# Optimization experiments

Measured on AMD Instinct MI355X. Metric: run time of the kernel, lower is better.

The kernel has to match this reference:

```python
import jax, jax.numpy as jnp
import numpy as np

B, S, D, H = 2, 4096, 512, 8
HD = D // H  # head_dim = 64


def setup_inputs() -> dict:
    key = jax.random.key(0)
    ks = jax.random.split(key, 12)
    scale = 0.02
    inp = {
        "q": jax.random.normal(ks[0], (B, S, D), dtype=jnp.float32),
        "k": jax.random.normal(ks[1], (B, S, D), dtype=jnp.float32),
        "v": jax.random.normal(ks[2], (B, S, D), dtype=jnp.float32),
        "mask": jax.random.randint(ks[3], (B, S, S), 0, 2, dtype=jnp.int32),
        "wq_kernel": jax.random.normal(ks[4], (D, D), dtype=jnp.float32) * scale,
        "wq_bias": jnp.zeros((D,), dtype=jnp.float32),
        "wk_kernel": jax.random.normal(ks[5], (D, D), dtype=jnp.float32) * scale,
        "wk_bias": jnp.zeros((D,), dtype=jnp.float32),
        "wv_kernel": jax.random.normal(ks[6], (D, D), dtype=jnp.float32) * scale,
        "wv_bias": jnp.zeros((D,), dtype=jnp.float32),
        "wo_kernel": jax.random.normal(ks[7], (D, D), dtype=jnp.float32) * scale,
        "wo_bias": jnp.zeros((D,), dtype=jnp.float32),
    }
    return inp


def reference(q, k, v, mask, wq_kernel, wq_bias, wk_kernel, wk_bias,
              wv_kernel, wv_bias, wo_kernel, wo_bias):
    # Dense projections
    qp = q @ wq_kernel + wq_bias            # [B,S,D]
    kp = k @ wk_kernel + wk_bias
    vp = v @ wv_kernel + wv_bias

    def split_heads(x):
        # [B,S,D] -> [B,H,S,HD]
        return x.reshape(B, S, H, HD).transpose(0, 2, 1, 3)

    qh, kh, vh = split_heads(qp), split_heads(kp), split_heads(vp)

    # Scaled dot-product attention (materializes full [B,H,S,S] scores,
    # faithful to the original unfused implementation's math)
    scores = jnp.einsum('bhqd,bhkd->bhqk', qh, kh) / jnp.sqrt(
        jnp.asarray(HD, dtype=jnp.float32))
    scores = scores + mask.astype(jnp.float32)[:, None, :, :] * (-1e9)
    attn = jax.nn.softmax(scores, axis=-1)
    out = jnp.einsum('bhqk,bhkd->bhqd', attn, vh)   # [B,H,S,HD]

    # merge heads: [B,H,S,HD] -> [B,S,D]
    out = out.transpose(0, 2, 1, 3).reshape(B, S, D)
    return out @ wo_kernel + wo_bias
```

## Files before the change

kernel.cpp:

```cpp
#include <hip/hip_runtime.h>
#include <stdint.h>

#define B_ 2
#define S_ 4096
#define D_ 512
#define H_ 8
#define HD_ 64
#define M_ (B_*S_)

typedef __attribute__((ext_vector_type(8))) short bf16x8;
typedef __attribute__((ext_vector_type(4))) float f32x4;

#define QSCALE (0.125f * 1.44269504088896341f)
#define MFMA16(A,B,C) __builtin_amdgcn_mfma_f32_16x16x32_bf16((A),(B),(C),0,0,0)

__device__ __forceinline__ unsigned short f2bf(float f) {
  union { float f; unsigned u; } un; un.f = f;
  unsigned u = un.u;
  return (unsigned short)((u + 0x7fffu + ((u >> 16) & 1u)) >> 16);
}

__device__ __forceinline__ unsigned cvtpk(float lo, float hi) {
  unsigned r;
  asm("v_cvt_pk_bf16_f32 %0, %1, %2" : "=v"(r) : "v"(lo), "v"(hi));
  return r;
}

__device__ __forceinline__ void gl16(const void* g, void* l) {
  __builtin_amdgcn_global_load_lds(
      (const __attribute__((address_space(1))) void*)g,
      (__attribute__((address_space(3))) void*)l, 16, 0, 0);
}

__device__ __forceinline__ int kperm_inv(int p) {
  return ((p & 0x1C) << 1) | ((p & 0x20) >> 3) | (p & 3);
}

__global__ __launch_bounds__(256) void wtrans4(const float* __restrict__ w0, const float* __restrict__ w1,
                                               const float* __restrict__ w2, const float* __restrict__ w3,
                                               unsigned short* __restrict__ t0, unsigned short* __restrict__ t1,
                                               unsigned short* __restrict__ t2, unsigned short* __restrict__ t3) {
  const float* W = blockIdx.z==0?w0: blockIdx.z==1?w1: blockIdx.z==2?w2:w3;
  unsigned short* T = blockIdx.z==0?t0: blockIdx.z==1?t1: blockIdx.z==2?t2:t3;
  __shared__ float tile[32][33];
  int n0 = blockIdx.x*32, k0 = blockIdx.y*32;
  int tx = threadIdx.x & 31, ty = threadIdx.x >> 5;
  #pragma unroll
  for (int i=0;i<4;i++)
    tile[ty + i*8][tx] = W[(size_t)(k0 + ty + i*8)*D_ + n0 + tx];
  __syncthreads();
  #pragma unroll
  for (int i=0;i<4;i++)
    T[(size_t)(n0 + ty + i*8)*D_ + k0 + tx] = f2bf(tile[tx][ty + i*8]);
}

template<int OUT_MODE, int CONVA>
__device__ __forceinline__ void gemm_body(const void* __restrict__ Ap,
                                          const unsigned short* __restrict__ Wt,
                                          const float* __restrict__ bias,
                                          void* __restrict__ Out, float oscale) {
  __shared__ __align__(16) unsigned short lAB[2*128*64];
  unsigned short* lA = lAB;
  unsigned short* lB = lAB + 128*64;
  int bm = blockIdx.x, bn = blockIdx.y;
  int tid = threadIdx.x, lane = tid & 63, wid = tid >> 6;
  int g = lane >> 4, cc = lane & 15;
  int wm = wid >> 1, wn = wid & 1;

  f32x4 acc[4][4];
  #pragma unroll
  for (int mi=0;mi<4;mi++)
    #pragma unroll
    for (int ni=0;ni<4;ni++)
      acc[mi][ni] = (f32x4){0.f,0.f,0.f,0.f};

  for (int ks = 0; ks < D_; ks += 64) {
    __syncthreads();
    #pragma unroll
    for (int c4 = 0; c4 < 4; c4++) {
      int idx = wid*256 + c4*64 + lane;
      int row = idx >> 3, ch = idx & 7;
      int sw = ch ^ (row & 7);
      bf16x8 va;
      if (CONVA) {
        const float* a32 = (const float*)Ap + (size_t)(bm*128 + row)*D_ + ks + ch*8;
        float4 f0 = *(const float4*)a32;
        float4 f1 = *(const float4*)(a32 + 4);
        union { unsigned d[4]; bf16x8 v; } u;
        u.d[0] = cvtpk(f0.x, f0.y);
        u.d[1] = cvtpk(f0.z, f0.w);
        u.d[2] = cvtpk(f1.x, f1.y);
        u.d[3] = cvtpk(f1.z, f1.w);
        va = u.v;
      } else {
        va = *(const bf16x8*)((const unsigned short*)Ap + (size_t)(bm*128 + row)*D_ + ks + ch*8);
      }
      bf16x8 vb = *(const bf16x8*)(Wt + (size_t)(bn*128 + row)*D_ + ks + ch*8);
      *(bf16x8*)((char*)lA + row*128 + sw*16) = va;
      *(bf16x8*)((char*)lB + row*128 + sw*16) = vb;
    }
    __syncthreads();
    #pragma unroll
    for (int kk = 0; kk < 2; kk++) {
      bf16x8 af[4], bfv[4];
      #pragma unroll
      for (int mi=0;mi<4;mi++) {
        int row = wm*64 + mi*16 + cc;
        af[mi] = *(const bf16x8*)((const char*)lA + row*128 + (((4*kk+g) ^ (row&7))<<4));
      }
      #pragma unroll
      for (int ni=0;ni<4;ni++) {
        int row = wn*64 + ni*16 + cc;
        bfv[ni] = *(const bf16x8*)((const char*)lB + row*128 + (((4*kk+g) ^ (row&7))<<4));
      }
      #pragma unroll
      for (int mi=0;mi<4;mi++)
        #pragma unroll
        for (int ni=0;ni<4;ni++)
          acc[mi][ni] = MFMA16(af[mi], bfv[ni], acc[mi][ni]);
    }
  }

  if (OUT_MODE == 2) {
    __syncthreads();
    char* ldsT = (char*)lAB + wid*8192;
    #pragma unroll
    for (int ni=0;ni<4;ni++) {
      int n_l = ni*16 + cc;
      float bv = bias[bn*128 + wn*64 + n_l];
      #pragma unroll
      for (int mi=0;mi<4;mi++) {
        ushort4 pk;
        pk.x = f2bf(acc[mi][ni][0] + bv);
        pk.y = f2bf(acc[mi][ni][1] + bv);
        pk.z = f2bf(acc[mi][ni][2] + bv);
        pk.w = f2bf(acc[mi][ni][3] + bv);
        *(ushort4*)(ldsT + n_l*128 + ((32*mi + 8*g) ^ ((n_l&7)<<4))) = pk;
      }
    }
    asm volatile("s_waitcnt lgkmcnt(0)" ::: "memory");
    __builtin_amdgcn_sched_barrier(0);
    #pragma unroll
    for (int it=0; it<8; ++it) {
      int task = it*64 + lane;
      int row = task >> 3, ch = task & 7;
      bf16x8 vv = *(const bf16x8*)(ldsT + row*128 + ((ch ^ (row&7))<<4));
      int n_g = bn*128 + wn*64 + row;
      int m_g = bm*128 + wm*64 + ch*8;
      int bb = m_g >> 12, ss = m_g & (S_-1);
      int hh = n_g >> 6, hd = n_g & 63;
      *(bf16x8*)((unsigned short*)Out + (((size_t)(bb*H_+hh)*HD_ + hd)*S_ + ss)) = vv;
    }
    return;
  }

  #pragma unroll
  for (int ni=0;ni<4;ni++) {
    int n = bn*128 + wn*64 + ni*16 + cc;
    float bv = bias[n];
    #pragma unroll
    for (int mi=0;mi<4;mi++) {
      f32x4 vacc = acc[mi][ni];
      #pragma unroll
      for (int j=0;j<4;j++) {
        int r = bm*128 + wm*64 + mi*16 + 4*g + j;
        float val = (vacc[j] + bv) * oscale;
        if (OUT_MODE == 0) {
          int b = r >> 12, s = r & (S_-1);
          int h = n >> 6, hd = n & 63;
          ((unsigned short*)Out)[(((size_t)(b*H_ + h)*S_ + s) << 6) + hd] = f2bf(val);
        } else {
          ((float*)Out)[(size_t)r*D_ + n] = val;
        }
      }
    }
  }
}

__global__ __launch_bounds__(256,3) void qkv_gemm(
    const float* __restrict__ q32, const float* __restrict__ k32, const float* __restrict__ v32,
    const unsigned short* __restrict__ wqt, const unsigned short* __restrict__ wkt,
    const unsigned short* __restrict__ wvt,
    const float* __restrict__ bq, const float* __restrict__ bk, const float* __restrict__ bv,
    unsigned short* __restrict__ Qp, unsigned short* __restrict__ Kp,
    unsigned short* __restrict__ Vt,
    const int* __restrict__ mask, unsigned long long* __restrict__ bits) {
  if (blockIdx.z == 0) {
    const int lin = blockIdx.x + (blockIdx.y << 6);
    const int wid = threadIdx.x >> 6, lane = threadIdx.x & 63;
    const int wave_g = lin*4 + wid;
    const int* mp = mask + (size_t)wave_g*512*64 + lane;
    unsigned long long* bp = bits + (size_t)wave_g*512;
    #pragma unroll 1
    for (int it = 0; it < 64; ++it) {
      int m0 = mp[(it*8+0)*64]; int m1 = mp[(it*8+1)*64];
      int m2 = mp[(it*8+2)*64]; int m3 = mp[(it*8+3)*64];
      int m4 = mp[(it*8+4)*64]; int m5 = mp[(it*8+5)*64];
      int m6 = mp[(it*8+6)*64]; int m7 = mp[(it*8+7)*64];
      unsigned long long b0 = __ballot(m0 != 0);
      unsigned long long b1 = __ballot(m1 != 0);
      unsigned long long b2 = __ballot(m2 != 0);
      unsigned long long b3 = __ballot(m3 != 0);
      unsigned long long b4 = __ballot(m4 != 0);
      unsigned long long b5 = __ballot(m5 != 0);
      unsigned long long b6 = __ballot(m6 != 0);
      unsigned long long b7 = __ballot(m7 != 0);
      if (lane == 0) {
        bp[it*8+0] = b0; bp[it*8+1] = b1; bp[it*8+2] = b2; bp[it*8+3] = b3;
        bp[it*8+4] = b4; bp[it*8+5] = b5; bp[it*8+6] = b6; bp[it*8+7] = b7;
      }
    }
    return;
  }
  if (blockIdx.z == 1)      gemm_body<0,1>(q32, wqt, bq, Qp, QSCALE);
  else if (blockIdx.z == 2) gemm_body<0,1>(k32, wkt, bk, Kp, 1.0f);
  else                      gemm_body<2,1>(v32, wvt, bv, Vt, 1.0f);
}

__global__ __launch_bounds__(256,3) void o_gemm(const unsigned short* __restrict__ att,
                                                const unsigned short* __restrict__ wot,
                                                const float* __restrict__ bo,
                                                float* __restrict__ out) {
  gemm_body<1,0>(att, wot, bo, out, 1.0f);
}


#define WAITBAR { asm volatile("s_waitcnt vmcnt(6)" ::: "memory"); \
                  __builtin_amdgcn_s_barrier(); }

#define ISSUE(SLOT, TIDX) { \
    int tn_ = (TIDX) < NT ? (TIDX) : NT-1; \
    char* kb_ = lds + (SLOT)*8192 + woff; \
    char* vb_ = lds + 32768 + (SLOT)*8192 + woff; \
    gl16(gkA + (size_t)tn_*(64*HD_), kb_); \
    gl16(gkB + (size_t)tn_*(64*HD_), kb_ + 4096); \
    gl16(gvA + tn_*64, vb_); \
    gl16(gvB + tn_*64, vb_ + 4096); \
    msk0[SLOT] = mb0p[tn_]; \
    msk1[SLOT] = mb1p[tn_]; }

#define QK(SLOT, S0, S1) { \
    __builtin_amdgcn_s_setprio(1); \
    _Pragma("unroll") \
    for (int t4=0;t4<4;t4++) { \
      bf16x8 ak0 = *(const bf16x8*)(lds + (SLOT)*8192 + rdO[t4][0]); \
      bf16x8 ak1 = *(const bf16x8*)(lds + (SLOT)*8192 + rdO[t4][1]); \
      f32x4 s0 = (f32x4){0.f,0.f,0.f,0.f}; \
      s0 = MFMA16(ak0, aq00, s0); \
      s0 = MFMA16(ak1, aq01, s0); \
      f32x4 s1 = (f32x4){0.f,0.f,0.f,0.f}; \
      s1 = MFMA16(ak0, aq10, s1); \
      s1 = MFMA16(ak1, aq11, s1); \
      S0[t4] = s0; S1[t4] = s1; \
    } \
    __builtin_amdgcn_s_setprio(0); }

#define SMPV(S0, S1, VSLOT, MSLOT) { \
    unsigned long long sh0 = msk0[MSLOT] >> g8, sh1 = msk1[MSLOT] >> g8; \
    unsigned lo0=(unsigned)sh0, hi0=(unsigned)(sh0>>32); \
    unsigned lo1=(unsigned)sh1, hi1=(unsigned)(sh1>>32); \
    union { unsigned d[2][4]; bf16x8 v[2]; } P0_, P1_; \
    _Pragma("unroll") \
    for (int t4=0;t4<4;t4++) { \
      unsigned bm0=(t4&1)?hi0:lo0, bm1=(t4&1)?hi1:lo1; \
      const int bb=(t4>>1)*4; \
      float a0=__builtin_amdgcn_exp2f(S0[t4][0]-mj); \
      float a1=__builtin_amdgcn_exp2f(S0[t4][1]-mj); \
      float a2=__builtin_amdgcn_exp2f(S0[t4][2]-mj); \
      float a3=__builtin_amdgcn_exp2f(S0[t4][3]-mj); \
      a0=(bm0&(1u<<(bb+0)))?0.f:a0; a1=(bm0&(1u<<(bb+1)))?0.f:a1; \
      a2=(bm0&(1u<<(bb+2)))?0.f:a2; a3=(bm0&(1u<<(bb+3)))?0.f:a3; \
      P0_.d[t4&1][(t4>>1)*2]   = cvtpk(a0,a1); \
      P0_.d[t4&1][(t4>>1)*2+1] = cvtpk(a2,a3); \
      float c0=__builtin_amdgcn_exp2f(S1[t4][0]-mj); \
      float c1=__builtin_amdgcn_exp2f(S1[t4][1]-mj); \
      float c2=__builtin_amdgcn_exp2f(S1[t4][2]-mj); \
      float c3=__builtin_amdgcn_exp2f(S1[t4][3]-mj); \
      c0=(bm1&(1u<<(bb+0)))?0.f:c0; c1=(bm1&(1u<<(bb+1)))?0.f:c1; \
      c2=(bm1&(1u<<(bb+2)))?0.f:c2; c3=(bm1&(1u<<(bb+3)))?0.f:c3; \
      P1_.d[t4&1][(t4>>1)*2]   = cvtpk(c0,c1); \
      P1_.d[t4&1][(t4>>1)*2+1] = cvtpk(c2,c3); \
    } \
    __builtin_amdgcn_s_setprio(1); \
    _Pragma("unroll") \
    for (int kk=0;kk<2;kk++) { \
      lj40 = MFMA16(P0_.v[kk], vones, lj40); \
      lj41 = MFMA16(P1_.v[kk], vones, lj41); \
      _Pragma("unroll") \
      for (int t4=0;t4<4;t4++) { \
        bf16x8 bv8 = *(const bf16x8*)(lds + 32768 + (VSLOT)*8192 + rdO[t4][kk]); \
        o20[t4] = MFMA16(P0_.v[kk], bv8, o20[t4]); \
        o21[t4] = MFMA16(P1_.v[kk], bv8, o21[t4]); \
      } \
    } \
    __builtin_amdgcn_s_setprio(0); \
    float pm0 = fmaxf(fmaxf(fmaxf(S0[0][0],S0[0][1]),fmaxf(S0[0][2],S0[0][3])),  \
                fmaxf(fmaxf(fmaxf(S0[1][0],S0[1][1]),fmaxf(S0[1][2],S0[1][3])),  \
                fmaxf(fmaxf(fmaxf(S0[2][0],S0[2][1]),fmaxf(S0[2][2],S0[2][3])),  \
                      fmaxf(fmaxf(S0[3][0],S0[3][1]),fmaxf(S0[3][2],S0[3][3]))))); \
    float pm1 = fmaxf(fmaxf(fmaxf(S1[0][0],S1[0][1]),fmaxf(S1[0][2],S1[0][3])),  \
                fmaxf(fmaxf(fmaxf(S1[1][0],S1[1][1]),fmaxf(S1[1][2],S1[1][3])),  \
                fmaxf(fmaxf(fmaxf(S1[2][0],S1[2][1]),fmaxf(S1[2][2],S1[2][3])),  \
                      fmaxf(fmaxf(S1[3][0],S1[3][1]),fmaxf(S1[3][2],S1[3][3]))))); \
    float pm = fmaxf(pm0, pm1); \
    if (__any(pm > mj + 7.f)) { \
      pm = fmaxf(pm, __shfl_xor(pm, 16)); \
      pm = fmaxf(pm, __shfl_xor(pm, 32)); \
      float mn = fmaxf(mj, pm); \
      float alpha = __builtin_amdgcn_exp2f(mj - mn); \
      mj = mn; \
      _Pragma("unroll") \
      for (int j=0;j<4;j++) { \
        float aj = __shfl(alpha, 4*g + j); \
        lj40[j] *= aj; lj41[j] *= aj; \
        _Pragma("unroll") \
        for (int t4=0;t4<4;t4++) { o20[t4][j] *= aj; o21[t4][j] *= aj; } \
      } \
    } }

__global__ __launch_bounds__(256,2) void fattn(const unsigned short* __restrict__ Qp,
                                               const unsigned short* __restrict__ Kp,
                                               const unsigned short* __restrict__ Vt,
                                               const unsigned long long* __restrict__ bits,
                                               unsigned short* __restrict__ attO) {
  __shared__ __align__(16) char lds[65536];
  const int tid = threadIdx.x, lane = tid & 63, wid = tid >> 6;
  const int g = lane >> 4, cc = lane & 15;
  const int g8 = g << 3;

  const int n = blockIdx.x;
  const int xcd = n & 7, idx = n >> 3;
  const int bh = xcd*2 + (idx >> 5);
  const int qb = idx & 31;
  const int b = bh >> 3;
  const int q0w = qb*128 + wid*32;

  const unsigned short* Qb = Qp + (size_t)bh*S_*HD_;
  const unsigned short* Kb = Kp + (size_t)bh*S_*HD_;
  const unsigned short* Vb = Vt + (size_t)bh*HD_*S_;

  bf16x8 aq00 = *(const bf16x8*)(Qb + (size_t)(q0w+cc)*HD_ + g8);
  bf16x8 aq01 = *(const bf16x8*)(Qb + (size_t)(q0w+cc)*HD_ + 32 + g8);
  bf16x8 aq10 = *(const bf16x8*)(Qb + (size_t)(q0w+16+cc)*HD_ + g8);
  bf16x8 aq11 = *(const bf16x8*)(Qb + (size_t)(q0w+16+cc)*HD_ + 32 + g8);

  int rdO[4][2];
  #pragma unroll
  for (int t4=0;t4<4;t4++) {
    int row = t4*16 + cc;
    int base = row*128 + ((g ^ (row&7)) << 4);
    rdO[t4][0] = base;
    rdO[t4][1] = base ^ 64;
  }

  const int p0 = wid*8 + (lane >> 3);
  const int sl = lane & 7;
  const int cK = sl ^ (p0 & 7);
  const unsigned short* gkA = Kb + (size_t)kperm_inv(p0)      *HD_ + cK*8;
  const unsigned short* gkB = Kb + (size_t)kperm_inv(p0 + 32) *HD_ + cK*8;
  const unsigned short* gvA = Vb + (size_t)p0*S_ + cK*8;
  const unsigned short* gvB = gvA + (size_t)32*S_;
  const int woff = wid*1024;

  const unsigned long long* mb0p = bits + ((size_t)(b*S_ + q0w +      cc)) * (S_/64);
  const unsigned long long* mb1p = bits + ((size_t)(b*S_ + q0w + 16 + cc)) * (S_/64);

  union { unsigned d[4]; bf16x8 v; } onesu;
  onesu.d[0] = onesu.d[1] = onesu.d[2] = onesu.d[3] = 0x3F803F80u;
  const bf16x8 vones = onesu.v;

  f32x4 o20[4], o21[4];
  #pragma unroll
  for (int t4=0;t4<4;t4++) { o20[t4] = (f32x4){0.f,0.f,0.f,0.f}; o21[t4] = (f32x4){0.f,0.f,0.f,0.f}; }
  f32x4 lj40 = (f32x4){0.f,0.f,0.f,0.f};
  f32x4 lj41 = (f32x4){0.f,0.f,0.f,0.f};
  float mj = 0.f;

  unsigned long long msk0[4], msk1[4];
  f32x4 stA0[4], stA1[4], stB0[4], stB1[4];

  const int NT = S_/64;

  ISSUE(0, 0)
  ISSUE(1, 1)

  WAITBAR ISSUE(2, 2) QK(0, stA0, stA1)
  WAITBAR ISSUE(3, 3) QK(1, stB0, stB1) SMPV(stA0, stA1, 0, 0)
  WAITBAR ISSUE(0, 4) QK(2, stA0, stA1) SMPV(stB0, stB1, 1, 1)
  WAITBAR ISSUE(1, 5) QK(3, stB0, stB1) SMPV(stA0, stA1, 2, 2)

  #pragma unroll 1
  for (int t = 4; t < NT; t += 4) {
    WAITBAR ISSUE(2, t+2) QK(0, stA0, stA1) SMPV(stB0, stB1, 3, 3)
    WAITBAR ISSUE(3, t+3) QK(1, stB0, stB1) SMPV(stA0, stA1, 0, 0)
    WAITBAR ISSUE(0, t+4) QK(2, stA0, stA1) SMPV(stB0, stB1, 1, 1)
    WAITBAR ISSUE(1, t+5) QK(3, stB0, stB1) SMPV(stA0, stA1, 2, 2)
  }

  SMPV(stB0, stB1, 3, 3)

  const int h = bh & (H_-1);
  #pragma unroll
  for (int j=0;j<4;j++) {
    float i0 = __builtin_amdgcn_rcpf(lj40[j]);
    float i1 = __builtin_amdgcn_rcpf(lj41[j]);
    int qr0 = q0w + 4*g + j;
    int qr1 = q0w + 16 + 4*g + j;
    unsigned short* orow0 = attO + ((size_t)b*S_ + qr0)*D_ + h*HD_;
    unsigned short* orow1 = attO + ((size_t)b*S_ + qr1)*D_ + h*HD_;
    #pragma unroll
    for (int t4=0;t4<4;t4++) {
      orow0[t4*16 + cc] = f2bf(o20[t4][j] * i0);
      orow1[t4*16 + cc] = f2bf(o21[t4][j] * i1);
    }
  }
}

extern "C" void kernel_launch(void* const* d_in, const int* in_sizes, int n_in,
                              void* d_out, int out_size, void* d_ws, size_t ws_size,
                              hipStream_t stream) {
  const float* q    = (const float*)d_in[0];
  const float* k    = (const float*)d_in[1];
  const float* v    = (const float*)d_in[2];
  const int*   mask = (const int*)  d_in[3];
  const float* wq   = (const float*)d_in[4];
  const float* bq   = (const float*)d_in[5];
  const float* wk   = (const float*)d_in[6];
  const float* bk   = (const float*)d_in[7];
  const float* wv   = (const float*)d_in[8];
  const float* bv   = (const float*)d_in[9];
  const float* wo   = (const float*)d_in[10];
  const float* bo   = (const float*)d_in[11];

  char* ws = (char*)d_ws;
  const size_t SZ_MAT = (size_t)M_ * D_ * 2;
  const size_t SZ_W   = (size_t)D_ * D_ * 2;
  unsigned short* wqt = (unsigned short*)(ws);
  unsigned short* wkt = (unsigned short*)(ws + SZ_W);
  unsigned short* wvt = (unsigned short*)(ws + 2*SZ_W);
  unsigned short* wot = (unsigned short*)(ws + 3*SZ_W);
  unsigned short* Qp  = (unsigned short*)(ws + 4*SZ_W);
  unsigned short* Kp  = (unsigned short*)(ws + 4*SZ_W + SZ_MAT);
  unsigned short* Vt  = (unsigned short*)(ws + 4*SZ_W + 2*SZ_MAT);
  unsigned short* att = (unsigned short*)(ws + 4*SZ_W + 3*SZ_MAT);
  unsigned long long* bits = (unsigned long long*)(ws + 4*SZ_W + 4*SZ_MAT);

  wtrans4<<<dim3(16,16,4), 256, 0, stream>>>(wq, wk, wv, wo, wqt, wkt, wvt, wot);
  qkv_gemm<<<dim3(64,4,4), 256, 0, stream>>>(q, k, v, wqt, wkt, wvt,
                                             bq, bk, bv, Qp, Kp, Vt, mask, bits);
  fattn<<<512, 256, 0, stream>>>(Qp, Kp, Vt, bits, att);
  o_gemm<<<dim3(64,4), 256, 0, stream>>>(att, wot, bo, (float*)d_out);
}
```

Before: 182.6 us.

## Split attention KV range across two blocks and merge with combine kernel

The flash attention kernel now splits each query block's key range into two halves handled by separate blocks (1024 blocks instead of 512). Each block writes unnormalized fp32 partial outputs, row sums and running maxima, and a new combine kernel rescales and merges them into bf16 attention output. The LDS pipeline shrinks from four slots to double buffering with a full vmcnt(0) wait, halving LDS so occupancy can rise to four blocks per CU. This adds an extra kernel launch and fp32 partial-buffer traffic, and weakens load/compute overlap in exchange for more parallelism.

```diff
diff --git a/kernel.cpp b/kernel.cpp
--- a/kernel.cpp
+++ b/kernel.cpp
@@ -7,6 +7,7 @@
 #define H_ 8
 #define HD_ 64
 #define M_ (B_*S_)
+#define NROW 65536
 
 typedef __attribute__((ext_vector_type(8))) short bf16x8;
 typedef __attribute__((ext_vector_type(4))) float f32x4;
@@ -225,38 +226,34 @@
 }
 
 
-#define WAITBAR { asm volatile("s_waitcnt vmcnt(6)" ::: "memory"); \
-                  __builtin_amdgcn_s_barrier(); }
-
-#define ISSUE(SLOT, TIDX) { \
-    int tn_ = (TIDX) < NT ? (TIDX) : NT-1; \
-    char* kb_ = lds + (SLOT)*8192 + woff; \
-    char* vb_ = lds + 32768 + (SLOT)*8192 + woff; \
-    gl16(gkA + (size_t)tn_*(64*HD_), kb_); \
-    gl16(gkB + (size_t)tn_*(64*HD_), kb_ + 4096); \
-    gl16(gvA + tn_*64, vb_); \
-    gl16(gvB + tn_*64, vb_ + 4096); \
-    msk0[SLOT] = mb0p[tn_]; \
-    msk1[SLOT] = mb1p[tn_]; }
-
-#define QK(SLOT, S0, S1) { \
+#define FA_ISSUE(NCUR, MN0, MN1) { \
+    char* kb_ = lds + (NCUR)*8192 + woff; \
+    char* vb_ = lds + 16384 + (NCUR)*8192 + woff; \
+    gl16(gkA, kb_); gl16(gkB, kb_ + 4096); \
+    gl16(gvA, vb_); gl16(gvB, vb_ + 4096); \
+    gkA += 64*HD_; gkB += 64*HD_; gvA += 64; gvB += 64; \
+    MN0 = *mb0p++; MN1 = *mb1p++; }
+
+#define FA_TILE(CUR, MC0, MC1, DOISSUE, MN0, MN1) { \
+    asm volatile("s_waitcnt vmcnt(0)" ::: "memory"); \
+    __builtin_amdgcn_s_barrier(); \
+    if (DOISSUE) FA_ISSUE((CUR)^1, MN0, MN1) \
+    f32x4 st0[4], st1[4]; \
     __builtin_amdgcn_s_setprio(1); \
     _Pragma("unroll") \
     for (int t4=0;t4<4;t4++) { \
-      bf16x8 ak0 = *(const bf16x8*)(lds + (SLOT)*8192 + rdO[t4][0]); \
-      bf16x8 ak1 = *(const bf16x8*)(lds + (SLOT)*8192 + rdO[t4][1]); \
+      bf16x8 ak0 = *(const bf16x8*)(lds + (CUR)*8192 + rdO[t4][0]); \
+      bf16x8 ak1 = *(const bf16x8*)(lds + (CUR)*8192 + rdO[t4][1]); \
       f32x4 s0 = (f32x4){0.f,0.f,0.f,0.f}; \
       s0 = MFMA16(ak0, aq00, s0); \
       s0 = MFMA16(ak1, aq01, s0); \
       f32x4 s1 = (f32x4){0.f,0.f,0.f,0.f}; \
       s1 = MFMA16(ak0, aq10, s1); \
       s1 = MFMA16(ak1, aq11, s1); \
-      S0[t4] = s0; S1[t4] = s1; \
+      st0[t4] = s0; st1[t4] = s1; \
     } \
-    __builtin_amdgcn_s_setprio(0); }
-
-#define SMPV(S0, S1, VSLOT, MSLOT) { \
-    unsigned long long sh0 = msk0[MSLOT] >> g8, sh1 = msk1[MSLOT] >> g8; \
+    __builtin_amdgcn_s_setprio(0); \
+    unsigned long long sh0 = (MC0) >> g8, sh1 = (MC1) >> g8; \
     unsigned lo0=(unsigned)sh0, hi0=(unsigned)(sh0>>32); \
     unsigned lo1=(unsigned)sh1, hi1=(unsigned)(sh1>>32); \
     union { unsigned d[2][4]; bf16x8 v[2]; } P0_, P1_; \
@@ -264,18 +261,18 @@
     for (int t4=0;t4<4;t4++) { \
       unsigned bm0=(t4&1)?hi0:lo0, bm1=(t4&1)?hi1:lo1; \
       const int bb=(t4>>1)*4; \
-      float a0=__builtin_amdgcn_exp2f(S0[t4][0]-mj); \
-      float a1=__builtin_amdgcn_exp2f(S0[t4][1]-mj); \
-      float a2=__builtin_amdgcn_exp2f(S0[t4][2]-mj); \
-      float a3=__builtin_amdgcn_exp2f(S0[t4][3]-mj); \
+      float a0=__builtin_amdgcn_exp2f(st0[t4][0]-mj); \
+      float a1=__builtin_amdgcn_exp2f(st0[t4][1]-mj); \
+      float a2=__builtin_amdgcn_exp2f(st0[t4][2]-mj); \
+      float a3=__builtin_amdgcn_exp2f(st0[t4][3]-mj); \
       a0=(bm0&(1u<<(bb+0)))?0.f:a0; a1=(bm0&(1u<<(bb+1)))?0.f:a1; \
       a2=(bm0&(1u<<(bb+2)))?0.f:a2; a3=(bm0&(1u<<(bb+3)))?0.f:a3; \
       P0_.d[t4&1][(t4>>1)*2]   = cvtpk(a0,a1); \
       P0_.d[t4&1][(t4>>1)*2+1] = cvtpk(a2,a3); \
-      float c0=__builtin_amdgcn_exp2f(S1[t4][0]-mj); \
-      float c1=__builtin_amdgcn_exp2f(S1[t4][1]-mj); \
-      float c2=__builtin_amdgcn_exp2f(S1[t4][2]-mj); \
-      float c3=__builtin_amdgcn_exp2f(S1[t4][3]-mj); \
+      float c0=__builtin_amdgcn_exp2f(st1[t4][0]-mj); \
+      float c1=__builtin_amdgcn_exp2f(st1[t4][1]-mj); \
+      float c2=__builtin_amdgcn_exp2f(st1[t4][2]-mj); \
+      float c3=__builtin_amdgcn_exp2f(st1[t4][3]-mj); \
       c0=(bm1&(1u<<(bb+0)))?0.f:c0; c1=(bm1&(1u<<(bb+1)))?0.f:c1; \
       c2=(bm1&(1u<<(bb+2)))?0.f:c2; c3=(bm1&(1u<<(bb+3)))?0.f:c3; \
       P1_.d[t4&1][(t4>>1)*2]   = cvtpk(c0,c1); \
@@ -288,20 +285,20 @@
       lj41 = MFMA16(P1_.v[kk], vones, lj41); \
       _Pragma("unroll") \
       for (int t4=0;t4<4;t4++) { \
-        bf16x8 bv8 = *(const bf16x8*)(lds + 32768 + (VSLOT)*8192 + rdO[t4][kk]); \
+        bf16x8 bv8 = *(const bf16x8*)(lds + 16384 + (CUR)*8192 + rdO[t4][kk]); \
         o20[t4] = MFMA16(P0_.v[kk], bv8, o20[t4]); \
         o21[t4] = MFMA16(P1_.v[kk], bv8, o21[t4]); \
       } \
     } \
     __builtin_amdgcn_s_setprio(0); \
-    float pm0 = fmaxf(fmaxf(fmaxf(S0[0][0],S0[0][1]),fmaxf(S0[0][2],S0[0][3])),  \
-                fmaxf(fmaxf(fmaxf(S0[1][0],S0[1][1]),fmaxf(S0[1][2],S0[1][3])),  \
-                fmaxf(fmaxf(fmaxf(S0[2][0],S0[2][1]),fmaxf(S0[2][2],S0[2][3])),  \
-                      fmaxf(fmaxf(S0[3][0],S0[3][1]),fmaxf(S0[3][2],S0[3][3]))))); \
-    float pm1 = fmaxf(fmaxf(fmaxf(S1[0][0],S1[0][1]),fmaxf(S1[0][2],S1[0][3])),  \
-                fmaxf(fmaxf(fmaxf(S1[1][0],S1[1][1]),fmaxf(S1[1][2],S1[1][3])),  \
-                fmaxf(fmaxf(fmaxf(S1[2][0],S1[2][1]),fmaxf(S1[2][2],S1[2][3])),  \
-                      fmaxf(fmaxf(S1[3][0],S1[3][1]),fmaxf(S1[3][2],S1[3][3]))))); \
+    float pm0 = fmaxf(fmaxf(fmaxf(st0[0][0],st0[0][1]),fmaxf(st0[0][2],st0[0][3])),  \
+                fmaxf(fmaxf(fmaxf(st0[1][0],st0[1][1]),fmaxf(st0[1][2],st0[1][3])),  \
+                fmaxf(fmaxf(fmaxf(st0[2][0],st0[2][1]),fmaxf(st0[2][2],st0[2][3])),  \
+                      fmaxf(fmaxf(st0[3][0],st0[3][1]),fmaxf(st0[3][2],st0[3][3]))))); \
+    float pm1 = fmaxf(fmaxf(fmaxf(st1[0][0],st1[0][1]),fmaxf(st1[0][2],st1[0][3])),  \
+                fmaxf(fmaxf(fmaxf(st1[1][0],st1[1][1]),fmaxf(st1[1][2],st1[1][3])),  \
+                fmaxf(fmaxf(fmaxf(st1[2][0],st1[2][1]),fmaxf(st1[2][2],st1[2][3])),  \
+                      fmaxf(fmaxf(st1[3][0],st1[3][1]),fmaxf(st1[3][2],st1[3][3]))))); \
     float pm = fmaxf(pm0, pm1); \
     if (__any(pm > mj + 7.f)) { \
       pm = fmaxf(pm, __shfl_xor(pm, 16)); \
@@ -318,26 +315,29 @@
       } \
     } }
 
-__global__ __launch_bounds__(256,2) void fattn(const unsigned short* __restrict__ Qp,
-                                               const unsigned short* __restrict__ Kp,
-                                               const unsigned short* __restrict__ Vt,
-                                               const unsigned long long* __restrict__ bits,
-                                               unsigned short* __restrict__ attO) {
-  __shared__ __align__(16) char lds[65536];
+__global__ __launch_bounds__(256,4) void fattn_sk(const unsigned short* __restrict__ Qp,
+                                                  const unsigned short* __restrict__ Kp,
+                                                  const unsigned short* __restrict__ Vt,
+                                                  const unsigned long long* __restrict__ bits,
+                                                  float* __restrict__ opart,
+                                                  float* __restrict__ ljpart,
+                                                  float* __restrict__ mjpart) {
+  __shared__ __align__(16) char lds[32768];
   const int tid = threadIdx.x, lane = tid & 63, wid = tid >> 6;
   const int g = lane >> 4, cc = lane & 15;
   const int g8 = g << 3;
 
   const int n = blockIdx.x;
   const int xcd = n & 7, idx = n >> 3;
-  const int bh = xcd*2 + (idx >> 5);
-  const int qb = idx & 31;
+  const int half = idx & 1;
+  const int qb = (idx >> 1) & 31;
+  const int bh = xcd*2 + (idx >> 6);
   const int b = bh >> 3;
   const int q0w = qb*128 + wid*32;
 
   const unsigned short* Qb = Qp + (size_t)bh*S_*HD_;
-  const unsigned short* Kb = Kp + (size_t)bh*S_*HD_;
-  const unsigned short* Vb = Vt + (size_t)bh*HD_*S_;
+  const unsigned short* Kb = Kp + (size_t)bh*S_*HD_ + (size_t)half*2048*HD_;
+  const unsigned short* Vb = Vt + (size_t)bh*HD_*S_ + half*2048;
 
   bf16x8 aq00 = *(const bf16x8*)(Qb + (size_t)(q0w+cc)*HD_ + g8);
   bf16x8 aq01 = *(const bf16x8*)(Qb + (size_t)(q0w+cc)*HD_ + 32 + g8);
@@ -362,8 +362,8 @@
   const unsigned short* gvB = gvA + (size_t)32*S_;
   const int woff = wid*1024;
 
-  const unsigned long long* mb0p = bits + ((size_t)(b*S_ + q0w +      cc)) * (S_/64);
-  const unsigned long long* mb1p = bits + ((size_t)(b*S_ + q0w + 16 + cc)) * (S_/64);
+  const unsigned long long* mb0p = bits + ((size_t)(b*S_ + q0w +      cc)) * (S_/64) + half*32;
+  const unsigned long long* mb1p = bits + ((size_t)(b*S_ + q0w + 16 + cc)) * (S_/64) + half*32;
 
   union { unsigned d[4]; bf16x8 v; } onesu;
   onesu.d[0] = onesu.d[1] = onesu.d[2] = onesu.d[3] = 0x3F803F80u;
@@ -376,44 +376,67 @@
   f32x4 lj41 = (f32x4){0.f,0.f,0.f,0.f};
   float mj = 0.f;
 
-  unsigned long long msk0[4], msk1[4];
-  f32x4 stA0[4], stA1[4], stB0[4], stB1[4];
-
-  const int NT = S_/64;
-
-  ISSUE(0, 0)
-  ISSUE(1, 1)
-
-  WAITBAR ISSUE(2, 2) QK(0, stA0, stA1)
-  WAITBAR ISSUE(3, 3) QK(1, stB0, stB1) SMPV(stA0, stA1, 0, 0)
-  WAITBAR ISSUE(0, 4) QK(2, stA0, stA1) SMPV(stB0, stB1, 1, 1)
-  WAITBAR ISSUE(1, 5) QK(3, stB0, stB1) SMPV(stA0, stA1, 2, 2)
+  unsigned long long mA0=0, mA1=0, mB0=0, mB1=0;
+
+  const int NT = 32;
+
+  FA_ISSUE(0, mA0, mA1)
 
   #pragma unroll 1
-  for (int t = 4; t < NT; t += 4) {
-    WAITBAR ISSUE(2, t+2) QK(0, stA0, stA1) SMPV(stB0, stB1, 3, 3)
-    WAITBAR ISSUE(3, t+3) QK(1, stB0, stB1) SMPV(stA0, stA1, 0, 0)
-    WAITBAR ISSUE(0, t+4) QK(2, stA0, stA1) SMPV(stB0, stB1, 1, 1)
-    WAITBAR ISSUE(1, t+5) QK(3, stB0, stB1) SMPV(stA0, stA1, 2, 2)
-  }
-
-  SMPV(stB0, stB1, 3, 3)
-
-  const int h = bh & (H_-1);
+  for (int t2 = 0; t2 < NT; t2 += 2) {
+    FA_TILE(0, mA0, mA1, true,         mB0, mB1)
+    FA_TILE(1, mB0, mB1, (t2+2 < NT),  mA0, mA1)
+  }
+
+  const int rowb = bh*S_ + q0w;
+  float* op = opart + (size_t)half*NROW*64;
   #pragma unroll
   for (int j=0;j<4;j++) {
-    float i0 = __builtin_amdgcn_rcpf(lj40[j]);
-    float i1 = __builtin_amdgcn_rcpf(lj41[j]);
-    int qr0 = q0w + 4*g + j;
-    int qr1 = q0w + 16 + 4*g + j;
-    unsigned short* orow0 = attO + ((size_t)b*S_ + qr0)*D_ + h*HD_;
-    unsigned short* orow1 = attO + ((size_t)b*S_ + qr1)*D_ + h*HD_;
+    int qr0 = rowb + 4*g + j;
+    int qr1 = qr0 + 16;
     #pragma unroll
     for (int t4=0;t4<4;t4++) {
-      orow0[t4*16 + cc] = f2bf(o20[t4][j] * i0);
-      orow1[t4*16 + cc] = f2bf(o21[t4][j] * i1);
-    }
-  }
+      op[(size_t)qr0*64 + t4*16 + cc] = o20[t4][j];
+      op[(size_t)qr1*64 + t4*16 + cc] = o21[t4][j];
+    }
+    if (cc == 0) {
+      ljpart[half*NROW + qr0] = lj40[j];
+      ljpart[half*NROW + qr1] = lj41[j];
+    }
+  }
+  if (g == 0) {
+    mjpart[half*NROW + rowb + cc]      = mj;
+    mjpart[half*NROW + rowb + 16 + cc] = mj;
+  }
+}
+
+__global__ __launch_bounds__(256) void combine(const float* __restrict__ opart,
+                                               const float* __restrict__ ljpart,
+                                               const float* __restrict__ mjpart,
+                                               unsigned short* __restrict__ att) {
+  int idx = blockIdx.x*256 + threadIdx.x;
+  int row = idx >> 3;
+  int hd0 = (idx & 7) << 3;
+  float m0 = mjpart[row], m1 = mjpart[NROW + row];
+  float l0 = ljpart[row], l1 = ljpart[NROW + row];
+  float Mx = fmaxf(m0, m1);
+  float w0 = __builtin_amdgcn_exp2f(m0 - Mx);
+  float w1 = __builtin_amdgcn_exp2f(m1 - Mx);
+  float inv = 1.0f / (l0*w0 + l1*w1);
+  w0 *= inv; w1 *= inv;
+  const float4* p0 = (const float4*)(opart + (size_t)row*64 + hd0);
+  const float4* p1 = (const float4*)(opart + (size_t)NROW*64 + (size_t)row*64 + hd0);
+  float4 a0 = p0[0], a1 = p0[1];
+  float4 c0 = p1[0], c1 = p1[1];
+  int bh = row >> 12, q = row & (S_-1);
+  int bb = bh >> 3, h = bh & 7;
+  unsigned short* dst = att + ((size_t)(bb*S_ + q))*D_ + h*HD_ + hd0;
+  ushort4 r0 = { f2bf(a0.x*w0 + c0.x*w1), f2bf(a0.y*w0 + c0.y*w1),
+                 f2bf(a0.z*w0 + c0.z*w1), f2bf(a0.w*w0 + c0.w*w1) };
+  ushort4 r1 = { f2bf(a1.x*w0 + c1.x*w1), f2bf(a1.y*w0 + c1.y*w1),
+                 f2bf(a1.z*w0 + c1.z*w1), f2bf(a1.w*w0 + c1.w*w1) };
+  ((ushort4*)dst)[0] = r0;
+  ((ushort4*)dst)[1] = r1;
 }
 
 extern "C" void kernel_launch(void* const* d_in, const int* in_sizes, int n_in,
@@ -444,10 +467,15 @@
   unsigned short* Vt  = (unsigned short*)(ws + 4*SZ_W + 2*SZ_MAT);
   unsigned short* att = (unsigned short*)(ws + 4*SZ_W + 3*SZ_MAT);
   unsigned long long* bits = (unsigned long long*)(ws + 4*SZ_W + 4*SZ_MAT);
+  char* base2 = ws + 4*SZ_W + 4*SZ_MAT + 4*1024*1024;
+  float* opart  = (float*)base2;
+  float* ljpart = (float*)(base2 + (size_t)2*NROW*64*4);
+  float* mjpart = (float*)(base2 + (size_t)2*NROW*64*4 + 2*NROW*4);
 
   wtrans4<<<dim3(16,16,4), 256, 0, stream>>>(wq, wk, wv, wo, wqt, wkt, wvt, wot);
   qkv_gemm<<<dim3(64,4,4), 256, 0, stream>>>(q, k, v, wqt, wkt, wvt,
                                              bq, bk, bv, Qp, Kp, Vt, mask, bits);
-  fattn<<<512, 256, 0, stream>>>(Qp, Kp, Vt, bits, att);
+  fattn_sk<<<1024, 256, 0, stream>>>(Qp, Kp, Vt, bits, opart, ljpart, mjpart);
+  combine<<<2048, 256, 0, stream>>>(opart, ljpart, mjpart, att);
   o_gemm<<<dim3(64,4), 256, 0, stream>>>(att, wot, bo, (float*)d_out);
 }
```

Measured after the change: 281.8 us. 1.54x slower.
